# Optimization experiments

Hardware: AMD Instinct MI355X
Metric: run time of the kernel (lower is better)

The kernel has to match this reference:

```python
import jax, jax.numpy as jnp
import numpy as np

BATCH = 131072
NUM_OSC = 4
NUM_SPEC = 300
FREQ_LO, FREQ_HI = 0.5, 5.0


def setup_inputs() -> dict:
    key = jax.random.key(0)
    ks = jax.random.split(key, 8)
    return {
        "G": jax.random.normal(ks[0], (BATCH, 8), dtype=jnp.float32),
        "W1": jax.random.normal(ks[1], (100, 8), dtype=jnp.float32) * 0.3,
        "b1": jax.random.normal(ks[2], (100,), dtype=jnp.float32) * 0.1,
        "W2": jax.random.normal(ks[3], (100, 100), dtype=jnp.float32) * 0.1,
        "b2": jax.random.normal(ks[4], (100,), dtype=jnp.float32) * 0.1,
        "W_w0": jax.random.normal(ks[5], (NUM_OSC, 100), dtype=jnp.float32) * 0.1,
        "W_wp": jax.random.normal(ks[6], (NUM_OSC, 100), dtype=jnp.float32) * 0.1,
        # torch.nn.init.uniform_(lin_g.weight, a=0.0, b=0.1)
        "W_g": jax.random.uniform(ks[7], (NUM_OSC, 100), dtype=jnp.float32) * 0.1,
    }


def reference(G, W1, b1, W2, b2, W_w0, W_wp, W_g):
    # MLP trunk: 8 -> 100 -> 100, ReLU on both layers
    out = jax.nn.relu(G @ W1.T + b1)
    out = jax.nn.relu(out @ W2.T + b2)          # (B, 100)

    # Oscillator parameter heads (bias-free), ReLU-clamped, shape (B, 4, 1)
    w0 = jax.nn.relu(out @ W_w0.T)[:, :, None]
    wp = jax.nn.relu(out @ W_wp.T)[:, :, None]
    g = jax.nn.relu(out @ W_g.T)[:, :, None]

    # Frequency grid (300,) broadcast against (B, 4, 1)
    w = jnp.arange(FREQ_LO, FREQ_HI, (FREQ_HI - FREQ_LO) / NUM_SPEC, dtype=jnp.float32)

    # Lorentz oscillator imaginary permittivity
    num = (wp ** 2) * (w * g)                   # (B, 4, 300)
    den = (w0 ** 2 - w ** 2) ** 2 + (w ** 2) * (g ** 2)
    e2 = num / den
    return jnp.sum(e2, axis=1)                  # (B, 300)
```

## Files before the change

### kernel.cpp

```cpp
#include <hip/hip_runtime.h>

#define BATCH 131072
#define NS    300
#define H     100
#define BLK   512
#define EPB   256
#define NQ4   (EPB * NS / 4)

#define REP25(M) M(0) M(1) M(2) M(3) M(4) M(5) M(6) M(7) M(8) M(9) M(10) M(11) \
  M(12) M(13) M(14) M(15) M(16) M(17) M(18) M(19) M(20) M(21) M(22) M(23) M(24)

__device__ __forceinline__ float qswap1(float x) {
    return __int_as_float(__builtin_amdgcn_mov_dpp(__float_as_int(x), 0xB1, 0xF, 0xF, true));
}
__device__ __forceinline__ float qswap2(float x) {
    return __int_as_float(__builtin_amdgcn_mov_dpp(__float_as_int(x), 0x4E, 0xF, 0xF, true));
}

__global__ __launch_bounds__(BLK, 4)
void lorentz_fused(const float* __restrict__ G,  const float* __restrict__ W1,
                   const float* __restrict__ b1, const float* __restrict__ W2,
                   const float* __restrict__ b2, const float* __restrict__ Ww0,
                   const float* __restrict__ Wwp, const float* __restrict__ Wg,
                   float* __restrict__ out)
{
    __shared__ float4 sW2c4[H * 4 * 7];
    __shared__ float4 sHead4[H * 4];
    __shared__ float4 sP04[EPB], sP14[EPB], sP24[EPB];
    __shared__ float  sW1[H * 8];
    __shared__ float  sB1[H], sB2[H];

    const int tid = threadIdx.x;

    {
        float* sW2cF = (float*)sW2c4;
        for (int i = tid; i < H * H; i += BLK) {
            int j = i / 100, k = i - j * 100;
            int q = k / 25, kk = k - q * 25;
            sW2cF[(j * 4 + q) * 28 + kk] = W2[i];
        }
        for (int i = tid; i < H * 8; i += BLK) sW1[i] = W1[i];
        for (int i = tid; i < H; i += BLK) { sB1[i] = b1[i]; sB2[i] = b2[i]; }
        float* sHeadF = (float*)sHead4;
        for (int i = tid; i < H * 4; i += BLK) {
            int j = i >> 2, q = i & 3;
            sHeadF[i * 4 + 0] = Ww0[q * H + j];
            sHeadF[i * 4 + 1] = Wwp[q * H + j];
            sHeadF[i * 4 + 2] = Wg [q * H + j];
            sHeadF[i * 4 + 3] = 0.f;
        }
    }
    __syncthreads();

    const int q  = tid & 3;
    const int gi = tid >> 2;
    const int e0 = blockIdx.x * EPB + gi * 2;

    const float4* gp = (const float4*)(G + (size_t)e0 * 8);
    const float4 ga0 = gp[0], gb0 = gp[1];
    const float4 ga1 = gp[2], gb1 = gp[3];

#define H1DECL(i) float h1a_##i, h1b_##i;
    REP25(H1DECL)
#undef H1DECL
#define L1E(dst, ga, gb)                                                        \
        { float s0 = fmaf(ga.x, ra.x, bb);  float s1 = ga.y * ra.y;             \
          s0 = fmaf(ga.z, ra.z, s0);  s1 = fmaf(ga.w, ra.w, s1);                \
          s0 = fmaf(gb.x, rb.x, s0);  s1 = fmaf(gb.y, rb.y, s1);                \
          s0 = fmaf(gb.z, rb.z, s0);  s1 = fmaf(gb.w, rb.w, s1);                \
          dst = fmaxf(s0 + s1, 0.f); }
#define L1(i) { const float4* r = (const float4*)&sW1[(q * 25 + (i)) * 8];      \
        const float4 ra = r[0], rb = r[1];                                      \
        const float bb = sB1[q * 25 + (i)];                                     \
        L1E(h1a_##i, ga0, gb0)  L1E(h1b_##i, ga1, gb1) }
    REP25(L1)
#undef L1

    float aw0a = 0.f, awpa = 0.f, agga = 0.f;
    float aw0b = 0.f, awpb = 0.f, aggb = 0.f;

#pragma unroll 2
    for (int j = 0; j < H; ++j) {
        const int cb = (j * 4 + q) * 7;
        const float4 c0 = sW2c4[cb + 0], c1 = sW2c4[cb + 1], c2 = sW2c4[cb + 2],
                     c3 = sW2c4[cb + 3], c4 = sW2c4[cb + 4], c5 = sW2c4[cb + 5],
                     c6 = sW2c4[cb + 6];
        const float4 hv  = sHead4[j * 4 + q];
        const float  b2j = sB2[j];

        float pa = 0.f, pb = 0.f;
#define CH1(w, i) pa = fmaf(h1a_##i, w, pa); pb = fmaf(h1b_##i, w, pb);
#define CH(t, i0, i1, i2, i3)                                                   \
        CH1(c##t.x, i0) CH1(c##t.y, i1) CH1(c##t.z, i2) CH1(c##t.w, i3)
        CH(0, 0, 1, 2, 3)     CH(1, 4, 5, 6, 7)     CH(2, 8, 9, 10, 11)
        CH(3, 12, 13, 14, 15) CH(4, 16, 17, 18, 19) CH(5, 20, 21, 22, 23)
        CH1(c6.x, 24)
#undef CH
#undef CH1
        float sa = pa + qswap1(pa); sa += qswap2(sa);
        float sb = pb + qswap1(pb); sb += qswap2(sb);
        const float h2a = fmaxf(sa + b2j, 0.f);
        const float h2b = fmaxf(sb + b2j, 0.f);

        aw0a = fmaf(h2a, hv.x, aw0a); awpa = fmaf(h2a, hv.y, awpa); agga = fmaf(h2a, hv.z, agga);
        aw0b = fmaf(h2b, hv.x, aw0b); awpb = fmaf(h2b, hv.y, awpb); aggb = fmaf(h2b, hv.z, aggb);
    }

    {
        float* P0 = (float*)sP04; float* P1 = (float*)sP14; float* P2 = (float*)sP24;
#define EMIT(aw, ap, ag, e)                                                     \
        { const float w0 = fmaxf(aw, 0.f), wp = fmaxf(ap, 0.f), gg = fmaxf(ag, 0.f); \
          const int ix = (gi * 2 + (e)) * 4 + q;                                \
          P0[ix] = w0 * w0;  P1[ix] = gg * gg;  P2[ix] = wp * wp * gg; }
        EMIT(aw0a, awpa, agga, 0)
        EMIT(aw0b, awpb, aggb, 1)
#undef EMIT
    }
    __syncthreads();

    float4* out4 = (float4*)out;
    const size_t base4 = (size_t)blockIdx.x * NQ4;

#define SPEC(idx4)                                                              \
    {   const int e  = (idx4) / 75;                                             \
        const int k4 = (idx4) - e * 75;                                         \
        const float4 P0 = sP04[e], P1 = sP14[e], P2 = sP24[e];                  \
        const float kb = (float)(k4 << 2);                                      \
        float4 r; float* rp = (float*)&r;                                       \
        _Pragma("unroll")                                                       \
        for (int i = 0; i < 4; ++i) {                                           \
            const float w   = 0.5f + (kb + (float)i) * 0.015f;                  \
            const float wsq = w * w;                                            \
            const float t0 = P0.x - wsq, t1 = P0.y - wsq,                       \
                        t2 = P0.z - wsq, t3 = P0.w - wsq;                       \
            const float d0 = fmaf(t0, t0, wsq * P1.x);                          \
            const float d1 = fmaf(t1, t1, wsq * P1.y);                          \
            const float d2 = fmaf(t2, t2, wsq * P1.z);                          \
            const float d3 = fmaf(t3, t3, wsq * P1.w);                          \
            const float d01 = d0 * d1, d23 = d2 * d3;                           \
            const float D   = d01 * d23;                                        \
            const float n01 = fmaf(P2.y, d0, P2.x * d1);                        \
            const float n23 = fmaf(P2.w, d2, P2.z * d3);                        \
            const float N   = fmaf(n01, d23, n23 * d01);                        \
            rp[i] = w * (N * __builtin_amdgcn_rcpf(D));                         \
        }                                                                       \
        out4[base4 + (idx4)] = r; }

    for (int it = 0; it < NQ4 / BLK; ++it) {
        const int idx4 = it * BLK + tid;
        SPEC(idx4)
    }
    if (tid < NQ4 - (NQ4 / BLK) * BLK) {
        const int idx4 = (NQ4 / BLK) * BLK + tid;
        SPEC(idx4)
    }
#undef SPEC
}

extern "C" void kernel_launch(void* const* d_in, const int* in_sizes, int n_in,
                              void* d_out, int out_size, void* d_ws, size_t ws_size,
                              hipStream_t stream) {
    const float* G   = (const float*)d_in[0];
    const float* W1  = (const float*)d_in[1];
    const float* b1  = (const float*)d_in[2];
    const float* W2  = (const float*)d_in[3];
    const float* b2  = (const float*)d_in[4];
    const float* Ww0 = (const float*)d_in[5];
    const float* Wwp = (const float*)d_in[6];
    const float* Wg  = (const float*)d_in[7];
    float* out = (float*)d_out;

    dim3 grid(BATCH / EPB);
    dim3 block(BLK);
    lorentz_fused<<<grid, block, 0, stream>>>(G, W1, b1, W2, b2, Ww0, Wwp, Wg, out);
}
```

Baseline: 83.73 us.

## Shrink blocks to one element per thread group and alias shared buffers

Block size drops from 512 to 256 threads and elements per block from 256 to 64, so each 4-thread group now handles one batch element instead of two. W1 and the biases are read straight from global memory rather than staged in shared memory, and the P buffers alias the W2 staging area behind an extra barrier. The aim is more blocks and a different occupancy/register balance. The cost is that W2 and the head weights are staged into shared memory four times as often per element, and the layer-2 loop loses the reuse of each weight load across two elements.

```diff
diff --git a/kernel.cpp b/kernel.cpp
--- a/kernel.cpp
+++ b/kernel.cpp
@@ -3,8 +3,9 @@
 #define BATCH 131072
 #define NS    300
 #define H     100
-#define BLK   512
-#define EPB   256
+#define BLK   256
+#define EPB   64
+#define NBLK  (BATCH / EPB)
 #define NQ4   (EPB * NS / 4)
 
 #define REP25(M) M(0) M(1) M(2) M(3) M(4) M(5) M(6) M(7) M(8) M(9) M(10) M(11) \
@@ -17,18 +18,19 @@
     return __int_as_float(__builtin_amdgcn_mov_dpp(__float_as_int(x), 0x4E, 0xF, 0xF, true));
 }
 
-__global__ __launch_bounds__(BLK, 4)
-void lorentz_fused(const float* __restrict__ G,  const float* __restrict__ W1,
-                   const float* __restrict__ b1, const float* __restrict__ W2,
-                   const float* __restrict__ b2, const float* __restrict__ Ww0,
+__global__ __launch_bounds__(BLK, 2)
+void lorentz_fused(const float* __restrict__ G,   const float* __restrict__ W1,
+                   const float* __restrict__ b1,  const float* __restrict__ W2,
+                   const float* __restrict__ b2,  const float* __restrict__ Ww0,
                    const float* __restrict__ Wwp, const float* __restrict__ Wg,
                    float* __restrict__ out)
 {
-    __shared__ float4 sW2c4[H * 4 * 7];
-    __shared__ float4 sHead4[H * 4];
-    __shared__ float4 sP04[EPB], sP14[EPB], sP24[EPB];
-    __shared__ float  sW1[H * 8];
-    __shared__ float  sB1[H], sB2[H];
+    __shared__ __align__(16) char smem[51200];
+    float4* sW2c4  = (float4*)smem;
+    float4* sHead4 = (float4*)(smem + 44800);
+    float4* sP0    = (float4*)smem;
+    float4* sP1    = (float4*)(smem + 1024);
+    float4* sP2    = (float4*)(smem + 2048);
 
     const int tid = threadIdx.x;
 
@@ -39,8 +41,6 @@
             int q = k / 25, kk = k - q * 25;
             sW2cF[(j * 4 + q) * 28 + kk] = W2[i];
         }
-        for (int i = tid; i < H * 8; i += BLK) sW1[i] = W1[i];
-        for (int i = tid; i < H; i += BLK) { sB1[i] = b1[i]; sB2[i] = b2[i]; }
         float* sHeadF = (float*)sHead4;
         for (int i = tid; i < H * 4; i += BLK) {
             int j = i >> 2, q = i & 3;
@@ -53,68 +53,65 @@
     __syncthreads();
 
     const int q  = tid & 3;
-    const int gi = tid >> 2;
-    const int e0 = blockIdx.x * EPB + gi * 2;
+    const int el = tid >> 2;
+    const int e0 = blockIdx.x * EPB + el;
 
     const float4* gp = (const float4*)(G + (size_t)e0 * 8);
-    const float4 ga0 = gp[0], gb0 = gp[1];
-    const float4 ga1 = gp[2], gb1 = gp[3];
+    const float4 gA = gp[0], gB = gp[1];
 
-#define H1DECL(i) float h1a_##i, h1b_##i;
+#define H1DECL(i) float h1_##i;
     REP25(H1DECL)
 #undef H1DECL
-#define L1E(dst, ga, gb)                                                        \
-        { float s0 = fmaf(ga.x, ra.x, bb);  float s1 = ga.y * ra.y;             \
-          s0 = fmaf(ga.z, ra.z, s0);  s1 = fmaf(ga.w, ra.w, s1);                \
-          s0 = fmaf(gb.x, rb.x, s0);  s1 = fmaf(gb.y, rb.y, s1);                \
-          s0 = fmaf(gb.z, rb.z, s0);  s1 = fmaf(gb.w, rb.w, s1);                \
-          dst = fmaxf(s0 + s1, 0.f); }
-#define L1(i) { const float4* r = (const float4*)&sW1[(q * 25 + (i)) * 8];      \
+#define L1(i) { const float4* r = (const float4*)(W1 + (q * 25 + (i)) * 8);     \
         const float4 ra = r[0], rb = r[1];                                      \
-        const float bb = sB1[q * 25 + (i)];                                     \
-        L1E(h1a_##i, ga0, gb0)  L1E(h1b_##i, ga1, gb1) }
+        float s0 = fmaf(gA.x, ra.x, b1[q * 25 + (i)]);                          \
+        float s1 = gA.y * ra.y;                                                 \
+        s0 = fmaf(gA.z, ra.z, s0);  s1 = fmaf(gA.w, ra.w, s1);                  \
+        s0 = fmaf(gB.x, rb.x, s0);  s1 = fmaf(gB.y, rb.y, s1);                  \
+        s0 = fmaf(gB.z, rb.z, s0);  s1 = fmaf(gB.w, rb.w, s1);                  \
+        h1_##i = fmaxf(s0 + s1, 0.f); }
     REP25(L1)
 #undef L1
 
-    float aw0a = 0.f, awpa = 0.f, agga = 0.f;
-    float aw0b = 0.f, awpb = 0.f, aggb = 0.f;
+    float aw0 = 0.f, awp = 0.f, agg = 0.f;
 
-#pragma unroll 2
+#pragma unroll 1
     for (int j = 0; j < H; ++j) {
         const int cb = (j * 4 + q) * 7;
         const float4 c0 = sW2c4[cb + 0], c1 = sW2c4[cb + 1], c2 = sW2c4[cb + 2],
                      c3 = sW2c4[cb + 3], c4 = sW2c4[cb + 4], c5 = sW2c4[cb + 5],
                      c6 = sW2c4[cb + 6];
         const float4 hv  = sHead4[j * 4 + q];
-        const float  b2j = sB2[j];
+        const float  b2j = b2[j];
 
-        float pa = 0.f, pb = 0.f;
-#define CH1(w, i) pa = fmaf(h1a_##i, w, pa); pb = fmaf(h1b_##i, w, pb);
-#define CH(t, i0, i1, i2, i3)                                                   \
-        CH1(c##t.x, i0) CH1(c##t.y, i1) CH1(c##t.z, i2) CH1(c##t.w, i3)
-        CH(0, 0, 1, 2, 3)     CH(1, 4, 5, 6, 7)     CH(2, 8, 9, 10, 11)
-        CH(3, 12, 13, 14, 15) CH(4, 16, 17, 18, 19) CH(5, 20, 21, 22, 23)
-        CH1(c6.x, 24)
-#undef CH
-#undef CH1
+        float p0 = 0.f, p1 = 0.f, p2 = 0.f, p3 = 0.f;
+        p0 = fmaf(h1_0,  c0.x, p0); p1 = fmaf(h1_1,  c0.y, p1);
+        p2 = fmaf(h1_2,  c0.z, p2); p3 = fmaf(h1_3,  c0.w, p3);
+        p0 = fmaf(h1_4,  c1.x, p0); p1 = fmaf(h1_5,  c1.y, p1);
+        p2 = fmaf(h1_6,  c1.z, p2); p3 = fmaf(h1_7,  c1.w, p3);
+        p0 = fmaf(h1_8,  c2.x, p0); p1 = fmaf(h1_9,  c2.y, p1);
+        p2 = fmaf(h1_10, c2.z, p2); p3 = fmaf(h1_11, c2.w, p3);
+        p0 = fmaf(h1_12, c3.x, p0); p1 = fmaf(h1_13, c3.y, p1);
+        p2 = fmaf(h1_14, c3.z, p2); p3 = fmaf(h1_15, c3.w, p3);
+        p0 = fmaf(h1_16, c4.x, p0); p1 = fmaf(h1_17, c4.y, p1);
+        p2 = fmaf(h1_18, c4.z, p2); p3 = fmaf(h1_19, c4.w, p3);
+        p0 = fmaf(h1_20, c5.x, p0); p1 = fmaf(h1_21, c5.y, p1);
+        p2 = fmaf(h1_22, c5.z, p2); p3 = fmaf(h1_23, c5.w, p3);
+        p0 = fmaf(h1_24, c6.x, p0);
+
+        float pa = (p0 + p1) + (p2 + p3);
         float sa = pa + qswap1(pa); sa += qswap2(sa);
-        float sb = pb + qswap1(pb); sb += qswap2(sb);
-        const float h2a = fmaxf(sa + b2j, 0.f);
-        const float h2b = fmaxf(sb + b2j, 0.f);
+        const float h2 = fmaxf(sa + b2j, 0.f);
 
-        aw0a = fmaf(h2a, hv.x, aw0a); awpa = fmaf(h2a, hv.y, awpa); agga = fmaf(h2a, hv.z, agga);
-        aw0b = fmaf(h2b, hv.x, aw0b); awpb = fmaf(h2b, hv.y, awpb); aggb = fmaf(h2b, hv.z, aggb);
+        aw0 = fmaf(h2, hv.x, aw0); awp = fmaf(h2, hv.y, awp); agg = fmaf(h2, hv.z, agg);
     }
 
+    __syncthreads();
     {
-        float* P0 = (float*)sP04; float* P1 = (float*)sP14; float* P2 = (float*)sP24;
-#define EMIT(aw, ap, ag, e)                                                     \
-        { const float w0 = fmaxf(aw, 0.f), wp = fmaxf(ap, 0.f), gg = fmaxf(ag, 0.f); \
-          const int ix = (gi * 2 + (e)) * 4 + q;                                \
-          P0[ix] = w0 * w0;  P1[ix] = gg * gg;  P2[ix] = wp * wp * gg; }
-        EMIT(aw0a, awpa, agga, 0)
-        EMIT(aw0b, awpb, aggb, 1)
-#undef EMIT
+        float* P0 = (float*)sP0; float* P1 = (float*)sP1; float* P2 = (float*)sP2;
+        const float w0 = fmaxf(aw0, 0.f), wp = fmaxf(awp, 0.f), gg = fmaxf(agg, 0.f);
+        const int ix = el * 4 + q;
+        P0[ix] = w0 * w0;  P1[ix] = gg * gg;  P2[ix] = wp * wp * gg;
     }
     __syncthreads();
 
@@ -124,7 +121,7 @@
 #define SPEC(idx4)                                                              \
     {   const int e  = (idx4) / 75;                                             \
         const int k4 = (idx4) - e * 75;                                         \
-        const float4 P0 = sP04[e], P1 = sP14[e], P2 = sP24[e];                  \
+        const float4 P0 = sP0[e], P1 = sP1[e], P2 = sP2[e];                     \
         const float kb = (float)(k4 << 2);                                      \
         float4 r; float* rp = (float*)&r;                                       \
         _Pragma("unroll")                                                       \
@@ -170,7 +167,5 @@
     const float* Wg  = (const float*)d_in[7];
     float* out = (float*)d_out;
 
-    dim3 grid(BATCH / EPB);
-    dim3 block(BLK);
-    lorentz_fused<<<grid, block, 0, stream>>>(G, W1, b1, W2, b2, Ww0, Wwp, Wg, out);
+    lorentz_fused<<<NBLK, BLK, 0, stream>>>(G, W1, b1, W2, b2, Ww0, Wwp, Wg, out);
 }
```

Result: slower. 128.0 us (+52.8%).
